# Kernel optimization log

Measured on AMD Instinct MI355X. Metric: run time of the kernel, lower is better.

Reference implementation:

```python
import jax, jax.numpy as jnp
import numpy as np

B, N, F, H, K, C = 2048, 62, 512, 128, 2, 2
EPS_BN = 1e-5
EPS_NORM = 1e-10
N_TRIL = N * (N + 1) // 2  # 1953, tril_indices incl. diagonal
FC_SIZES = [H * N, H * N // 2, H * N // 4, H * N // 8, C]  # [7936,3968,1984,992,2]


def setup_inputs() -> dict:
    key = jax.random.key(0)
    ks = jax.random.split(key, 16)
    inp = {
        "x": jax.random.normal(ks[0], (B, N, F), jnp.float32),
        "edge_weight": jax.random.uniform(ks[1], (N_TRIL,), jnp.float32),
        "bn_gamma": jnp.ones((F,), jnp.float32),
        "bn_beta": jnp.zeros((F,), jnp.float32),
        # xavier_normal for SGConv lin
        "lin_w": jax.random.normal(ks[2], (H, F), jnp.float32) * (2.0 / (F + H)) ** 0.5,
        "lin_b": jnp.zeros((H,), jnp.float32),
    }
    for i in range(4):
        fan_in, fan_out = FC_SIZES[i], FC_SIZES[i + 1]
        inp[f"fc{i}_w"] = jax.random.normal(ks[3 + i], (fan_out, fan_in), jnp.float32) * (2.0 / (fan_in + fan_out)) ** 0.5
        inp[f"fc{i}_b"] = jnp.zeros((fan_out,), jnp.float32)
    return inp


def _normalized_adj(edge_weight):
    """Build symmetric dense adjacency from tril params, normalize_matrix
    (relu + sym deg-norm), then SGConv.norm (D^-1/2 A D^-1/2; self-loops are
    already on the diagonal so add_remaining_self_loops is a no-op)."""
    xs, ys = np.tril_indices(N)
    Wm = jnp.zeros((N, N), jnp.float32).at[xs, ys].set(edge_weight)
    Wm = Wm + Wm.T - jnp.diag(jnp.diag(Wm))
    A = jax.nn.relu(Wm)
    dinv = jax.lax.rsqrt(A.sum(1) + EPS_NORM)
    A = dinv[:, None] * A * dinv[None, :]
    # SGConv normalization: deg = scatter_add over rows -> row sums
    deg = A.sum(1)
    dis = jnp.where(deg > 0, deg ** -0.5, 0.0)
    return dis[:, None] * A * dis[None, :]


def reference(x, edge_weight, bn_gamma, bn_beta, lin_w, lin_b,
              fc0_w, fc0_b, fc1_w, fc1_b, fc2_w, fc2_b, fc3_w, fc3_b):
    A = _normalized_adj(edge_weight)  # [N, N], shared across batch
    # BatchNorm1d over feature channels, stats over (batch, node) dims (train mode)
    mean = x.mean((0, 1))
    var = x.var((0, 1))
    h = (x - mean) * jax.lax.rsqrt(var + EPS_BN) * bn_gamma + bn_beta  # [B,N,F]
    # K-hop SGConv propagation == dense matmul with shared normalized adjacency
    for _ in range(K):
        h = jnp.einsum('ij,bjf->bif', A, h)
    h = h @ lin_w.T + lin_b           # [B, N, H]
    h = h.reshape(B, N * H)           # node-major flatten, matches x.view(batch,-1)
    # dropout is identity in eval mode
    for W, b in ((fc0_w, fc0_b), (fc1_w, fc1_b), (fc2_w, fc2_b)):
        h = jax.nn.relu(h @ W.T + b)
    return h @ fc3_w.T + fc3_b        # [B, C]
```

## Files before the change

kernel.cpp:

```cpp
#include <hip/hip_runtime.h>

typedef _Float16 f16;
typedef __attribute__((ext_vector_type(4))) _Float16 f16x4;
typedef __attribute__((ext_vector_type(8))) _Float16 f16x8;
typedef __attribute__((ext_vector_type(4))) float f32x4;

#define DEVI static __device__ __forceinline__

DEVI void async_copy16(const f16* g, f16* l) {
  __builtin_amdgcn_global_load_lds(
      (const __attribute__((address_space(1))) void*)g,
      (__attribute__((address_space(3))) void*)l, 16, 0, 0);
}

#define MEMPIN asm volatile("" ::: "memory")
#define RBAR __builtin_amdgcn_s_barrier()

__global__ __launch_bounds__(1024) void k_adj(const float* __restrict__ ew, float* __restrict__ out)
{
  __shared__ float sW[62][64];
  __shared__ float sT[62][64];
  __shared__ float d[62];
  const int tid = threadIdx.x;
  for (int idx = tid; idx < 62 * 62; idx += 1024) {
    int i = idx / 62, j = idx % 62;
    float w = (j <= i) ? ew[i * (i + 1) / 2 + j] : ew[j * (j + 1) / 2 + i];
    sW[i][j] = fmaxf(w, 0.f);
  }
  __syncthreads();
  if (tid < 62) {
    float s = 0.f;
    for (int j = 0; j < 62; j++) s += sW[tid][j];
    d[tid] = rsqrtf(s + 1e-10f);
  }
  __syncthreads();
  for (int idx = tid; idx < 62 * 62; idx += 1024) {
    int i = idx / 62, j = idx % 62;
    sW[i][j] *= d[i] * d[j];
  }
  __syncthreads();
  if (tid < 62) {
    float s = 0.f;
    for (int j = 0; j < 62; j++) s += sW[tid][j];
    d[tid] = (s > 0.f) ? rsqrtf(s) : 0.f;
  }
  __syncthreads();
  for (int idx = tid; idx < 62 * 62; idx += 1024) {
    int i = idx / 62, j = idx % 62;
    sW[i][j] *= d[i] * d[j];
  }
  __syncthreads();
  for (int idx = tid; idx < 62 * 64; idx += 1024) {
    int i = idx >> 6, j = idx & 63;
    float s = 0.f;
    if (j < 62) {
      for (int k = 0; k < 62; k++) s += sW[i][k] * sW[k][j];
    }
    sT[i][j] = s;
    out[idx] = s;
  }
  __syncthreads();
  if (tid < 62) {
    float s = 0.f;
    for (int j = 0; j < 62; j++) s += sT[tid][j];
    out[62 * 64 + tid] = s;
  }
}

__global__ __launch_bounds__(1024) void k_bnstats(const float* __restrict__ X, float* __restrict__ part)
{
  const int tid = threadIdx.x;
  const int c4 = (tid & 127) << 2;
  const int rg = tid >> 7;
  float sx = 0, sy = 0, sz = 0, sw = 0, qx = 0, qy = 0, qz = 0, qw = 0;
  const long r0 = (long)blockIdx.x * 496 + rg;
  for (int i = 0; i < 62; i++) {
    const float4 v = *(const float4*)(X + (r0 + 8 * i) * 512 + c4);
    sx += v.x; sy += v.y; sz += v.z; sw += v.w;
    qx += v.x * v.x; qy += v.y * v.y; qz += v.z * v.z; qw += v.w * v.w;
  }
  __shared__ float red[1024][8];
  red[tid][0] = sx; red[tid][1] = sy; red[tid][2] = sz; red[tid][3] = sw;
  red[tid][4] = qx; red[tid][5] = qy; red[tid][6] = qz; red[tid][7] = qw;
  __syncthreads();
  if (tid < 128) {
    float acc8[8];
#pragma unroll
    for (int j = 0; j < 8; j++) acc8[j] = 0.f;
#pragma unroll
    for (int g = 0; g < 8; g++)
#pragma unroll
      for (int j = 0; j < 8; j++) acc8[j] += red[g * 128 + tid][j];
    float* p = part + (long)blockIdx.x * 1024;
#pragma unroll
    for (int j = 0; j < 4; j++) p[c4 + j] = acc8[j];
#pragma unroll
    for (int j = 0; j < 4; j++) p[512 + c4 + j] = acc8[4 + j];
  }
}

__global__ __launch_bounds__(512) void k_bnfin(const float* __restrict__ part, const float* __restrict__ g,
                                               const float* __restrict__ be, float* __restrict__ ssb)
{
  const int c = threadIdx.x;
  float s = 0.f, q = 0.f;
  for (int b = 0; b < 256; b++) {
    s += part[b * 1024 + c];
    q += part[b * 1024 + 512 + c];
  }
  const float inv = 1.f / 126976.f;
  const float mean = s * inv;
  const float var = q * inv - mean * mean;
  const float sc = g[c] * rsqrtf(var + 1e-5f);
  ssb[c] = sc;
  ssb[512 + c] = be[c] - mean * sc;
}

__global__ __launch_bounds__(256) void k_foldw1(const float* __restrict__ lw, const float* __restrict__ ssb,
                                                f16* __restrict__ w1h, float* __restrict__ b1p)
{
  const int h = blockIdx.x;
  const int tid = threadIdx.x;
  float partl = 0.f;
  for (int f = tid; f < 512; f += 256) {
    const float w = lw[h * 512 + f];
    w1h[h * 512 + f] = (f16)(w * ssb[f]);
    partl += w * ssb[512 + f];
  }
  __shared__ float red[256];
  red[tid] = partl;
  __syncthreads();
  for (int s = 128; s; s >>= 1) {
    if (tid < s) red[tid] += red[tid + s];
    __syncthreads();
  }
  if (tid == 0) b1p[h] = red[0];
}

__global__ __launch_bounds__(256) void k_cvtw(const float* __restrict__ src, f16* __restrict__ dst,
                                              int N, int K, int Npad, int Kpad)
{
  const long total4 = (long)Npad * Kpad / 4;
  const int kp4 = Kpad >> 2;
  for (long i = (long)blockIdx.x * 256 + threadIdx.x; i < total4; i += (long)gridDim.x * 256) {
    const long n = i / kp4;
    const int k = (int)(i % kp4) << 2;
    f16x4 h;
    if (n < N && k < K) {
      const float4 v = *(const float4*)(src + n * K + k);
      h[0] = (f16)v.x; h[1] = (f16)v.y; h[2] = (f16)v.z; h[3] = (f16)v.w;
    } else {
      h[0] = (f16)0.f; h[1] = (f16)0.f; h[2] = (f16)0.f; h[3] = (f16)0.f;
    }
    *(f16x4*)(dst + i * 4) = h;
  }
}

__global__ __launch_bounds__(256, 2) void k_linprop(
    const float* __restrict__ X, const f16* __restrict__ Bw,
    const float* __restrict__ A2, const float* __restrict__ b1p,
    const float* __restrict__ lb, f16* __restrict__ Z)
{
  __shared__ f16 smem[128 * 128];
  __shared__ float sA2[62 * 64];
  __shared__ float sR[62];
  __shared__ float sB1[128];
  __shared__ float sLB[128];
  f16* sA = smem;
  f16* sB = smem + 8192;
  const int tid = threadIdx.x;
  const int lane = tid & 63;
  const int wave = tid >> 6;
  const int wr = wave >> 1, wc = wave & 1;
  const long rowA0 = (long)blockIdx.x * 124;

  for (int i = tid; i < 992; i += 256)
    *(float4*)&sA2[i * 4] = *(const float4*)(A2 + i * 4);
  if (tid < 62) sR[tid] = A2[3968 + tid];
  if (tid < 128) sB1[tid] = b1p[tid];
  if (tid >= 128) sLB[tid - 128] = lb[tid - 128];

  const int srow = tid >> 3;
  const int scolb = (tid & 7) << 4;
  const int gcolb = scolb ^ ((srow & 7) << 4);
  const f16* gB = Bw + (long)srow * 512 + (gcolb >> 1);
  f16* lB = sB + srow * 64 + (scolb >> 1);

  const int ac4 = tid & 15;
  const int ar0 = tid >> 4;
  const int aswz = (ar0 & 7) << 4;
  char* lAbase = (char*)sA + ar0 * 128 + ((ac4 * 8) ^ aswz);

  const int frow = lane & 15;
  const int kb = (lane >> 4) << 4;
  const int rswz = (lane & 7) << 4;

  f32x4 acc[4][4] = {};

  for (int kt = 0; kt < 512; kt += 64) {
#pragma unroll
    for (int i = 0; i < 8; i++) {
      long rr = rowA0 + ar0 + 16 * i;
      if (rr > 126975) rr = 126975;
      const float4 v = *(const float4*)(X + rr * 512 + kt + ac4 * 4);
      f16x4 hh;
      hh[0] = (f16)v.x; hh[1] = (f16)v.y; hh[2] = (f16)v.z; hh[3] = (f16)v.w;
      *(f16x4*)(lAbase + 16 * i * 128) = hh;
    }
#pragma unroll
    for (int i = 0; i < 4; i++)
      async_copy16(gB + kt + (long)i * (32 * 512), lB + i * 2048);
    __syncthreads();
#pragma unroll
    for (int kk = 0; kk < 2; kk++) {
      f16x8 af[4], bf[4];
#pragma unroll
      for (int m = 0; m < 4; m++) {
        const int row = wr * 64 + m * 16 + frow;
        af[m] = *(const f16x8*)((const char*)sA + row * 128 + ((kk * 64 + kb) ^ rswz));
      }
#pragma unroll
      for (int n = 0; n < 4; n++) {
        const int row = wc * 64 + n * 16 + frow;
        bf[n] = *(const f16x8*)((const char*)sB + row * 128 + ((kk * 64 + kb) ^ rswz));
      }
#pragma unroll
      for (int m = 0; m < 4; m++)
#pragma unroll
        for (int n = 0; n < 4; n++)
          acc[m][n] = __builtin_amdgcn_mfma_f32_16x16x32_f16(af[m], bf[n], acc[m][n], 0, 0, 0);
    }
    __syncthreads();
  }

  const int crow = wr * 64 + ((lane >> 4) << 2);
  const int ccol = wc * 64 + (lane & 15);
#pragma unroll
  for (int n = 0; n < 4; n++)
#pragma unroll
    for (int m = 0; m < 4; m++)
#pragma unroll
      for (int r = 0; r < 4; r++)
        smem[(crow + m * 16 + r) * 128 + ccol + n * 16] = (f16)acc[m][n][r];
  __syncthreads();

  const int h = tid & 127;
  const int g = tid >> 7;
  float yc[62];
#pragma unroll
  for (int j = 0; j < 62; j++) yc[j] = (float)smem[(g * 62 + j) * 128 + h];
  const float bh1 = sB1[h];
  const float bh2 = sLB[h];
  f16* zp = Z + ((long)blockIdx.x * 2 + g) * 7936 + h;
  for (int n = 0; n < 62; n++) {
    float s = 0.f;
#pragma unroll
    for (int j = 0; j < 62; j++) s += sA2[n * 64 + j] * yc[j];
    zp[n * 128] = (f16)(s + sR[n] * bh1 + bh2);
  }
}

template <int LOOPN, int MT, int NT, int KS>
__global__ __launch_bounds__(512, 2) void k_fc8(
    const f16* __restrict__ A, const f16* __restrict__ Bw, f16* __restrict__ P,
    const int K, const int kslice, const int PLD)
{
  __shared__ f16 sA[2][256 * 64];
  __shared__ f16 sB[2][256 * 64];
  const int tid = threadIdx.x;
  const int bid = blockIdx.x;
  const int xcd = bid & 7, ii = bid >> 3;
  int nt, mt, ks;
  if constexpr (NT == 16) {
    nt = xcd * 2 + (ii & 1); mt = (ii >> 1) & (MT - 1); ks = ii >> 4;
  } else {
    nt = xcd; mt = ii & (MT - 1); ks = ii >> 3;
  }
  const long rowA0 = (long)mt * 256;
  const long rowB0 = (long)nt * 256;
  const long k0 = (long)ks * kslice;

  const int srow = tid >> 3;
  const int scolb = (tid & 7) << 4;
  const int gcolb = scolb ^ ((srow & 7) << 4);
  const f16* gA = A + (rowA0 + srow) * (long)K + k0 + (gcolb >> 1);
  const f16* gB = Bw + (rowB0 + srow) * (long)K + k0 + (gcolb >> 1);

#define SGA(d, q, kt) async_copy16(gA + (kt) + (long)(q) * 64 * K, &sA[d][0] + (q) * 4096 + tid * 8)
#define SGB(d, q, kt) async_copy16(gB + (kt) + (long)(q) * 64 * K, &sB[d][0] + (q) * 4096 + tid * 8)

  const int lane = tid & 63;
  const int wave = tid >> 6;
  const int wr = wave >> 2;
  const int wc = wave & 3;
  const int frow = lane & 15;
  const int kb = (lane >> 4) << 4;
  const int rsw = (frow & 7) << 4;

  f32x4 acc[8][4] = {};
  f16x8 af[4][2], bf[4][2];

#define RDA(d, mh) do { _Pragma("unroll") for (int m_ = 0; m_ < 4; m_++) {                      \
    const int row_ = wr * 128 + (mh) * 64 + m_ * 16 + frow;                                     \
    af[m_][0] = *(const f16x8*)((const char*)&sA[d][0] + row_ * 128 + (kb ^ rsw));              \
    af[m_][1] = *(const f16x8*)((const char*)&sA[d][0] + row_ * 128 + ((64 + kb) ^ rsw)); } } while (0)
#define RDB(d) do { _Pragma("unroll") for (int n_ = 0; n_ < 4; n_++) {                          \
    const int row_ = wc * 64 + n_ * 16 + frow;                                                  \
    bf[n_][0] = *(const f16x8*)((const char*)&sB[d][0] + row_ * 128 + (kb ^ rsw));              \
    bf[n_][1] = *(const f16x8*)((const char*)&sB[d][0] + row_ * 128 + ((64 + kb) ^ rsw)); } } while (0)
#define QUAD(mh, nh) do { _Pragma("unroll") for (int m_ = 0; m_ < 4; m_++)                      \
    _Pragma("unroll") for (int n_ = 0; n_ < 2; n_++) {                                          \
      acc[(mh)*4+m_][(nh)*2+n_] = __builtin_amdgcn_mfma_f32_16x16x32_f16(af[m_][0], bf[(nh)*2+n_][0], acc[(mh)*4+m_][(nh)*2+n_], 0, 0, 0); \
      acc[(mh)*4+m_][(nh)*2+n_] = __builtin_amdgcn_mfma_f32_16x16x32_f16(af[m_][1], bf[(nh)*2+n_][1], acc[(mh)*4+m_][(nh)*2+n_], 0, 0, 0); } } while (0)
#define VMW8 asm volatile("s_waitcnt vmcnt(8)" ::: "memory")
#define VMW0 asm volatile("s_waitcnt vmcnt(0)" ::: "memory")
#define PRIO1 __builtin_amdgcn_s_setprio(1)
#define PRIO0 __builtin_amdgcn_s_setprio(0)

  SGA(0, 0, 0); SGA(0, 2, 0); SGB(0, 0, 0); SGB(0, 1, 0);
  SGA(0, 1, 0); SGA(0, 3, 0); SGB(0, 2, 0); SGB(0, 3, 0);
  SGA(1, 0, 64); SGA(1, 2, 64); SGB(1, 0, 64); SGB(1, 1, 64);
  SGA(1, 1, 64); SGA(1, 3, 64); SGB(1, 2, 64); SGB(1, 3, 64);

  for (int t = 0; t < LOOPN; ++t) {
    const long kt2 = (long)(t + 1) * 128;
    VMW8; MEMPIN; RBAR; MEMPIN;
    RDA(0, 0); RDB(0);
    PRIO1; QUAD(0, 0); PRIO0;
    MEMPIN; RBAR; MEMPIN;
    SGA(0, 0, kt2); SGA(0, 2, kt2); SGB(0, 0, kt2); SGB(0, 1, kt2);
    QUAD(0, 1);
    RDA(0, 1);
    QUAD(1, 0);
    MEMPIN; RBAR; MEMPIN;
    SGA(0, 1, kt2); SGA(0, 3, kt2); SGB(0, 2, kt2); SGB(0, 3, kt2);
    QUAD(1, 1);
    VMW8; MEMPIN; RBAR; MEMPIN;
    RDA(1, 0); RDB(1);
    PRIO1; QUAD(0, 0); PRIO0;
    MEMPIN; RBAR; MEMPIN;
    SGA(1, 0, kt2 + 64); SGA(1, 2, kt2 + 64); SGB(1, 0, kt2 + 64); SGB(1, 1, kt2 + 64);
    QUAD(0, 1);
    RDA(1, 1);
    QUAD(1, 0);
    MEMPIN; RBAR; MEMPIN;
    SGA(1, 1, kt2 + 64); SGA(1, 3, kt2 + 64); SGB(1, 2, kt2 + 64); SGB(1, 3, kt2 + 64);
    QUAD(1, 1);
  }
  VMW8; MEMPIN; RBAR; MEMPIN;
  RDA(0, 0); RDB(0);
  PRIO1; QUAD(0, 0); QUAD(0, 1); PRIO0;
  RDA(0, 1);
  PRIO1; QUAD(1, 0); QUAD(1, 1); PRIO0;
  VMW0; MEMPIN; RBAR; MEMPIN;
  RDA(1, 0); RDB(1);
  PRIO1; QUAD(0, 0); QUAD(0, 1); PRIO0;
  RDA(1, 1);
  PRIO1; QUAD(1, 0); QUAD(1, 1); PRIO0;

  f16* Pp = P + (long)ks * 2048 * PLD;
#pragma unroll
  for (int mi = 0; mi < 8; mi++) {
    const long r0 = rowA0 + wr * 128 + (mi >> 2) * 64 + (mi & 3) * 16 + ((lane >> 4) << 2);
#pragma unroll
    for (int n = 0; n < 4; n++) {
      const long col = rowB0 + wc * 64 + n * 16 + (lane & 15);
#pragma unroll
      for (int r = 0; r < 4; r++)
        Pp[(r0 + r) * PLD + col] = (f16)acc[mi][n][r];
    }
  }
#undef SGA
#undef SGB
#undef RDA
#undef RDB
#undef QUAD
#undef VMW8
#undef VMW0
#undef PRIO1
#undef PRIO0
}

template <int S>
__global__ __launch_bounds__(256) void k_fixs(const f16* __restrict__ P, const float* __restrict__ b,
                                              f16* __restrict__ C, int N, int realN)
{
  const long total = 2048L * N;
  const int mask = N - 1;
  const long stride = (long)gridDim.x * 256 * 8;
  for (long i = ((long)blockIdx.x * 256 + threadIdx.x) * 8; i < total; i += stride) {
    float s[8];
#pragma unroll
    for (int j = 0; j < 8; j++) s[j] = 0.f;
#pragma unroll
    for (int ps = 0; ps < S; ps++) {
      const f16x8 p = *(const f16x8*)(P + (long)ps * total + i);
#pragma unroll
      for (int j = 0; j < 8; j++) s[j] += (float)p[j];
    }
    const int col = (int)(i & mask);
    f16x8 o;
#pragma unroll
    for (int j = 0; j < 8; j++) {
      const int c = col + j;
      const float bb = (c < realN) ? b[c] : 0.f;
      o[j] = (f16)fmaxf(s[j] + bb, 0.f);
    }
    *(f16x8*)(C + i) = o;
  }
}

template <int RELU, int KS>
__global__ __launch_bounds__(256, 2) void k_gemm_f16(
    const f16* __restrict__ A, const f16* __restrict__ B,
    const float* __restrict__ bias, f16* __restrict__ C,
    int N, int K, int realN)
{
  __shared__ f16 sA[128 * 64];
  __shared__ f16 sB[128 * 64];
  const int tid = threadIdx.x;
  const int lane = tid & 63;
  const int wave = tid >> 6;
  const int wr = wave >> 1, wc = wave & 1;
  const int bid = blockIdx.x;
  const int xcd = bid & 7, idx = bid >> 3;
  const long rowA0 = (long)(xcd * 2 + (idx & 1)) * 128;
  long rowB0;
  int ks;
  if constexpr (KS == 2) {
    rowB0 = (long)((idx >> 1) & 7) * 128;
    ks = idx >> 4;
  } else {
    rowB0 = (long)(idx >> 1) * 128;
    ks = 0;
  }
  const int kslice = K / KS;
  const long k0 = (long)ks * kslice;

  const int srow = tid >> 3;
  const int scolb = (tid & 7) << 4;
  const int gcolb = scolb ^ ((srow & 7) << 4);
  const f16* gA = A + (rowA0 + srow) * (long)K + k0 + (gcolb >> 1);
  const f16* gB = B + (rowB0 + srow) * (long)K + k0 + (gcolb >> 1);
  f16* lA = sA + srow * 64 + (scolb >> 1);
  f16* lB = sB + srow * 64 + (scolb >> 1);
  const long rstep = 32L * K;

  const int frow = lane & 15;
  const int kb = (lane >> 4) << 4;
  const int rswz = (lane & 7) << 4;

  f32x4 acc[4][4] = {};

  for (int kt = 0; kt < kslice; kt += 64) {
#pragma unroll
    for (int i = 0; i < 4; i++) {
      async_copy16(gA + kt + i * rstep, lA + i * 2048);
      async_copy16(gB + kt + i * rstep, lB + i * 2048);
    }
    __syncthreads();
#pragma unroll
    for (int kk = 0; kk < 2; kk++) {
      f16x8 af[4], bf[4];
#pragma unroll
      for (int m = 0; m < 4; m++) {
        const int row = wr * 64 + m * 16 + frow;
        af[m] = *(const f16x8*)((const char*)sA + row * 128 + ((kk * 64 + kb) ^ rswz));
      }
#pragma unroll
      for (int n = 0; n < 4; n++) {
        const int row = wc * 64 + n * 16 + frow;
        bf[n] = *(const f16x8*)((const char*)sB + row * 128 + ((kk * 64 + kb) ^ rswz));
      }
#pragma unroll
      for (int m = 0; m < 4; m++)
#pragma unroll
        for (int n = 0; n < 4; n++)
          acc[m][n] = __builtin_amdgcn_mfma_f32_16x16x32_f16(af[m], bf[n], acc[m][n], 0, 0, 0);
    }
    __syncthreads();
  }

  const int crow = wr * 64 + ((lane >> 4) << 2);
  const int ccol = wc * 64 + (lane & 15);
  if constexpr (KS == 1) {
#pragma unroll
    for (int n = 0; n < 4; n++) {
      const int col = (int)rowB0 + ccol + n * 16;
      const float bb = (col < realN) ? bias[col] : 0.f;
#pragma unroll
      for (int m = 0; m < 4; m++) {
        const long gr = rowA0 + crow + m * 16;
#pragma unroll
        for (int r = 0; r < 4; r++) {
          float v = acc[m][n][r] + bb;
          if (RELU) v = fmaxf(v, 0.f);
          C[(gr + r) * N + col] = (f16)v;
        }
      }
    }
  } else {
    f16* Pp = C + (long)ks * 2048 * N;
#pragma unroll
    for (int n = 0; n < 4; n++) {
      const long col = rowB0 + ccol + n * 16;
#pragma unroll
      for (int m = 0; m < 4; m++) {
        const long gr = rowA0 + crow + m * 16;
#pragma unroll
        for (int r = 0; r < 4; r++)
          Pp[(gr + r) * N + col] = (f16)acc[m][n][r];
      }
    }
  }
}

__global__ __launch_bounds__(256) void k_fc3(const f16* __restrict__ H, const float* __restrict__ W,
                                             const float* __restrict__ b, float* __restrict__ out)
{
  const int row = blockIdx.x * 4 + (threadIdx.x >> 6);
  const int lane = threadIdx.x & 63;
  const f16* h = H + (long)row * 1024;
  float a0 = 0.f, a1 = 0.f;
  for (int k = lane; k < 992; k += 64) {
    const float v = (float)h[k];
    a0 += v * W[k];
    a1 += v * W[992 + k];
  }
  for (int off = 32; off; off >>= 1) {
    a0 += __shfl_down(a0, off);
    a1 += __shfl_down(a1, off);
  }
  if (lane == 0) {
    out[row * 2 + 0] = a0 + b[0];
    out[row * 2 + 1] = a1 + b[1];
  }
}

extern "C" void kernel_launch(void* const* d_in, const int* in_sizes, int n_in,
                              void* d_out, int out_size, void* d_ws, size_t ws_size,
                              hipStream_t stream)
{
  const float* x    = (const float*)d_in[0];
  const float* ew   = (const float*)d_in[1];
  const float* bng  = (const float*)d_in[2];
  const float* bnb  = (const float*)d_in[3];
  const float* linw = (const float*)d_in[4];
  const float* linb = (const float*)d_in[5];
  const float* w0   = (const float*)d_in[6];
  const float* b0   = (const float*)d_in[7];
  const float* w1   = (const float*)d_in[8];
  const float* b1   = (const float*)d_in[9];
  const float* w2   = (const float*)d_in[10];
  const float* b2   = (const float*)d_in[11];
  const float* w3   = (const float*)d_in[12];
  const float* b3   = (const float*)d_in[13];
  float* out = (float*)d_out;
  char* ws = (char*)d_ws;

  constexpr size_t oA2  = 0;
  constexpr size_t oSS  = 16384;
  constexpr size_t oB1P = 20480;
  constexpr size_t oW1H = 20992;
  constexpr size_t oP   = 152064;
  constexpr size_t oACC = oP;
  constexpr size_t oZ   = 33706496;
  constexpr size_t oW0H = 66212352;
  constexpr size_t WS_NEED = 131224064;
  constexpr size_t oH0  = oZ;
  constexpr size_t oW1F = oZ + 16777216;
  constexpr size_t oH1  = 67260928;
  constexpr size_t oW2F = 75649536;
  constexpr size_t oH2  = 79843840;
  if (ws_size < WS_NEED) return;

  float* A2  = (float*)(ws + oA2);
  float* acc = (float*)(ws + oACC);
  float* ssb = (float*)(ws + oSS);
  float* b1p = (float*)(ws + oB1P);
  f16* w1h = (f16*)(ws + oW1H);
  f16* P   = (f16*)(ws + oP);
  f16* Z   = (f16*)(ws + oZ);
  f16* w0h = (f16*)(ws + oW0H);
  f16* h0  = (f16*)(ws + oH0);
  f16* w1f = (f16*)(ws + oW1F);
  f16* h1  = (f16*)(ws + oH1);
  f16* w2f = (f16*)(ws + oW2F);
  f16* h2  = (f16*)(ws + oH2);

  k_adj<<<1, 1024, 0, stream>>>(ew, A2);
  k_bnstats<<<256, 1024, 0, stream>>>(x, acc);
  k_bnfin<<<1, 512, 0, stream>>>(acc, bng, bnb, ssb);
  k_foldw1<<<128, 256, 0, stream>>>(linw, ssb, w1h, b1p);
  k_cvtw<<<1024, 256, 0, stream>>>(w0, w0h, 3968, 7936, 4096, 7936);
  k_linprop<<<1024, 256, 0, stream>>>(x, w1h, A2, b1p, linb, Z);
  k_fc8<30, 8, 16, 2><<<256, 512, 0, stream>>>(Z, w0h, P, 7936, 3968, 4096);
  k_fixs<2><<<2048, 256, 0, stream>>>(P, b0, h0, 4096, 3968);
  k_cvtw<<<512, 256, 0, stream>>>(w1, w1f, 1984, 3968, 2048, 4096);
  k_cvtw<<<256, 256, 0, stream>>>(w2, w2f, 992, 1984, 1024, 2048);
  k_fc8<7, 8, 8, 4><<<256, 512, 0, stream>>>(h0, w1f, P, 4096, 1024, 2048);
  k_fixs<4><<<1024, 256, 0, stream>>>(P, b1, h1, 2048, 1984);
  k_gemm_f16<1, 2><<<256, 256, 0, stream>>>(h1, w2f, b2, P, 1024, 2048, 992);
  k_fixs<2><<<512, 256, 0, stream>>>(P, b2, h2, 1024, 992);
  k_fc3<<<512, 256, 0, stream>>>(h2, w3, b3, out);
}
```

Before: 465.1 us.

## Merge small kernels into co-scheduled launches and fuse final split-K reduction into fc3

Merges the adjacency build into the BN-stats launch as an extra block, folds the fc0 weight conversion into the linprop launch as extra blocks, and merges the fc0 split-K fixup with the fc1/fc2 weight conversions into one launch. The last split-K reduction plus bias and ReLU is folded into the fc3 dot-product kernel, dropping one kernel and the h2 buffer. The aim is fewer launches and more overlap between independent work. The linprop launch bound changes to 3 blocks per SM, which may limit registers, and the BN kernel now reserves LDS for the adjacency arrays.

```diff
diff --git a/kernel.cpp b/kernel.cpp
--- a/kernel.cpp
+++ b/kernel.cpp
@@ -16,12 +16,45 @@
 #define MEMPIN asm volatile("" ::: "memory")
 #define RBAR __builtin_amdgcn_s_barrier()
 
-__global__ __launch_bounds__(1024) void k_adj(const float* __restrict__ ew, float* __restrict__ out)
-{
+__global__ __launch_bounds__(1024) void k_bnadj(const float* __restrict__ X, float* __restrict__ part,
+                                                const float* __restrict__ ew, float* __restrict__ A2out)
+{
+  __shared__ float red[1024][8];
   __shared__ float sW[62][64];
   __shared__ float sT[62][64];
   __shared__ float d[62];
   const int tid = threadIdx.x;
+
+  if (blockIdx.x < 256) {
+    const int c4 = (tid & 127) << 2;
+    const int rg = tid >> 7;
+    float sx = 0, sy = 0, sz = 0, sw = 0, qx = 0, qy = 0, qz = 0, qw = 0;
+    const long r0 = (long)blockIdx.x * 496 + rg;
+    for (int i = 0; i < 62; i++) {
+      const float4 v = *(const float4*)(X + (r0 + 8 * i) * 512 + c4);
+      sx += v.x; sy += v.y; sz += v.z; sw += v.w;
+      qx += v.x * v.x; qy += v.y * v.y; qz += v.z * v.z; qw += v.w * v.w;
+    }
+    red[tid][0] = sx; red[tid][1] = sy; red[tid][2] = sz; red[tid][3] = sw;
+    red[tid][4] = qx; red[tid][5] = qy; red[tid][6] = qz; red[tid][7] = qw;
+    __syncthreads();
+    if (tid < 128) {
+      float acc8[8];
+#pragma unroll
+      for (int j = 0; j < 8; j++) acc8[j] = 0.f;
+#pragma unroll
+      for (int g = 0; g < 8; g++)
+#pragma unroll
+        for (int j = 0; j < 8; j++) acc8[j] += red[g * 128 + tid][j];
+      float* p = part + (long)blockIdx.x * 1024;
+#pragma unroll
+      for (int j = 0; j < 4; j++) p[c4 + j] = acc8[j];
+#pragma unroll
+      for (int j = 0; j < 4; j++) p[512 + c4 + j] = acc8[4 + j];
+    }
+    return;
+  }
+
   for (int idx = tid; idx < 62 * 62; idx += 1024) {
     int i = idx / 62, j = idx % 62;
     float w = (j <= i) ? ew[i * (i + 1) / 2 + j] : ew[j * (j + 1) / 2 + i];
@@ -57,45 +90,13 @@
       for (int k = 0; k < 62; k++) s += sW[i][k] * sW[k][j];
     }
     sT[i][j] = s;
-    out[idx] = s;
+    A2out[idx] = s;
   }
   __syncthreads();
   if (tid < 62) {
     float s = 0.f;
     for (int j = 0; j < 62; j++) s += sT[tid][j];
-    out[62 * 64 + tid] = s;
-  }
-}
-
-__global__ __launch_bounds__(1024) void k_bnstats(const float* __restrict__ X, float* __restrict__ part)
-{
-  const int tid = threadIdx.x;
-  const int c4 = (tid & 127) << 2;
-  const int rg = tid >> 7;
-  float sx = 0, sy = 0, sz = 0, sw = 0, qx = 0, qy = 0, qz = 0, qw = 0;
-  const long r0 = (long)blockIdx.x * 496 + rg;
-  for (int i = 0; i < 62; i++) {
-    const float4 v = *(const float4*)(X + (r0 + 8 * i) * 512 + c4);
-    sx += v.x; sy += v.y; sz += v.z; sw += v.w;
-    qx += v.x * v.x; qy += v.y * v.y; qz += v.z * v.z; qw += v.w * v.w;
-  }
-  __shared__ float red[1024][8];
-  red[tid][0] = sx; red[tid][1] = sy; red[tid][2] = sz; red[tid][3] = sw;
-  red[tid][4] = qx; red[tid][5] = qy; red[tid][6] = qz; red[tid][7] = qw;
-  __syncthreads();
-  if (tid < 128) {
-    float acc8[8];
-#pragma unroll
-    for (int j = 0; j < 8; j++) acc8[j] = 0.f;
-#pragma unroll
-    for (int g = 0; g < 8; g++)
-#pragma unroll
-      for (int j = 0; j < 8; j++) acc8[j] += red[g * 128 + tid][j];
-    float* p = part + (long)blockIdx.x * 1024;
-#pragma unroll
-    for (int j = 0; j < 4; j++) p[c4 + j] = acc8[j];
-#pragma unroll
-    for (int j = 0; j < 4; j++) p[512 + c4 + j] = acc8[4 + j];
+    A2out[62 * 64 + tid] = s;
   }
 }
 
@@ -137,12 +138,12 @@
   if (tid == 0) b1p[h] = red[0];
 }
 
-__global__ __launch_bounds__(256) void k_cvtw(const float* __restrict__ src, f16* __restrict__ dst,
-                                              int N, int K, int Npad, int Kpad)
+DEVI void cvt_body(const float* __restrict__ src, f16* __restrict__ dst,
+                   int N, int K, int Npad, int Kpad, int bix, int nblk)
 {
   const long total4 = (long)Npad * Kpad / 4;
   const int kp4 = Kpad >> 2;
-  for (long i = (long)blockIdx.x * 256 + threadIdx.x; i < total4; i += (long)gridDim.x * 256) {
+  for (long i = (long)bix * 256 + threadIdx.x; i < total4; i += (long)nblk * 256) {
     const long n = i / kp4;
     const int k = (int)(i % kp4) << 2;
     f16x4 h;
@@ -156,16 +157,23 @@
   }
 }
 
-__global__ __launch_bounds__(256, 2) void k_linprop(
+__global__ __launch_bounds__(256, 3) void k_linprop_cvt(
     const float* __restrict__ X, const f16* __restrict__ Bw,
     const float* __restrict__ A2, const float* __restrict__ b1p,
-    const float* __restrict__ lb, f16* __restrict__ Z)
+    const float* __restrict__ lb, f16* __restrict__ Z,
+    const float* __restrict__ w0, f16* __restrict__ w0h)
 {
   __shared__ f16 smem[128 * 128];
   __shared__ float sA2[62 * 64];
   __shared__ float sR[62];
   __shared__ float sB1[128];
   __shared__ float sLB[128];
+
+  if (blockIdx.x >= 1024) {
+    cvt_body(w0, w0h, 3968, 7936, 4096, 7936, blockIdx.x - 1024, 1024);
+    return;
+  }
+
   f16* sA = smem;
   f16* sB = smem + 8192;
   const int tid = threadIdx.x;
@@ -382,13 +390,13 @@
 }
 
 template <int S>
-__global__ __launch_bounds__(256) void k_fixs(const f16* __restrict__ P, const float* __restrict__ b,
-                                              f16* __restrict__ C, int N, int realN)
+DEVI void fix_body(const f16* __restrict__ P, const float* __restrict__ b,
+                   f16* __restrict__ C, int N, int realN, int bix, int nblk)
 {
   const long total = 2048L * N;
   const int mask = N - 1;
-  const long stride = (long)gridDim.x * 256 * 8;
-  for (long i = ((long)blockIdx.x * 256 + threadIdx.x) * 8; i < total; i += stride) {
+  const long stride = (long)nblk * 256 * 8;
+  for (long i = ((long)bix * 256 + threadIdx.x) * 8; i < total; i += stride) {
     float s[8];
 #pragma unroll
     for (int j = 0; j < 8; j++) s[j] = 0.f;
@@ -408,6 +416,24 @@
     }
     *(f16x8*)(C + i) = o;
   }
+}
+
+template <int S>
+__global__ __launch_bounds__(256) void k_fixs(const f16* __restrict__ P, const float* __restrict__ b,
+                                              f16* __restrict__ C, int N, int realN)
+{
+  fix_body<S>(P, b, C, N, realN, blockIdx.x, gridDim.x);
+}
+
+__global__ __launch_bounds__(256) void k_fixcvt(const f16* __restrict__ P, const float* __restrict__ b0,
+                                                f16* __restrict__ h0,
+                                                const float* __restrict__ w1, f16* __restrict__ w1f,
+                                                const float* __restrict__ w2, f16* __restrict__ w2f)
+{
+  const int bx = blockIdx.x;
+  if (bx < 2048)       fix_body<2>(P, b0, h0, 4096, 3968, bx, 2048);
+  else if (bx < 2560)  cvt_body(w1, w1f, 1984, 3968, 2048, 4096, bx - 2048, 512);
+  else                 cvt_body(w2, w2f, 992, 1984, 1024, 2048, bx - 2560, 256);
 }
 
 template <int RELU, int KS>
@@ -515,15 +541,17 @@
   }
 }
 
-__global__ __launch_bounds__(256) void k_fc3(const f16* __restrict__ H, const float* __restrict__ W,
-                                             const float* __restrict__ b, float* __restrict__ out)
+__global__ __launch_bounds__(256) void k_fc3p(const f16* __restrict__ P, const float* __restrict__ b2,
+                                              const float* __restrict__ W, const float* __restrict__ b,
+                                              float* __restrict__ out)
 {
   const int row = blockIdx.x * 4 + (threadIdx.x >> 6);
   const int lane = threadIdx.x & 63;
-  const f16* h = H + (long)row * 1024;
+  const f16* p0 = P + (long)row * 1024;
+  const f16* p1 = P + 2048L * 1024 + (long)row * 1024;
   float a0 = 0.f, a1 = 0.f;
   for (int k = lane; k < 992; k += 64) {
-    const float v = (float)h[k];
+    const float v = fmaxf((float)p0[k] + (float)p1[k] + b2[k], 0.f);
     a0 += v * W[k];
     a1 += v * W[992 + k];
   }
@@ -571,7 +599,6 @@
   constexpr size_t oW1F = oZ + 16777216;
   constexpr size_t oH1  = 67260928;
   constexpr size_t oW2F = 75649536;
-  constexpr size_t oH2  = 79843840;
   if (ws_size < WS_NEED) return;
 
   float* A2  = (float*)(ws + oA2);
@@ -586,21 +613,15 @@
   f16* w1f = (f16*)(ws + oW1F);
   f16* h1  = (f16*)(ws + oH1);
   f16* w2f = (f16*)(ws + oW2F);
-  f16* h2  = (f16*)(ws + oH2);
-
-  k_adj<<<1, 1024, 0, stream>>>(ew, A2);
-  k_bnstats<<<256, 1024, 0, stream>>>(x, acc);
+
+  k_bnadj<<<257, 1024, 0, stream>>>(x, acc, ew, A2);
   k_bnfin<<<1, 512, 0, stream>>>(acc, bng, bnb, ssb);
   k_foldw1<<<128, 256, 0, stream>>>(linw, ssb, w1h, b1p);
-  k_cvtw<<<1024, 256, 0, stream>>>(w0, w0h, 3968, 7936, 4096, 7936);
-  k_linprop<<<1024, 256, 0, stream>>>(x, w1h, A2, b1p, linb, Z);
+  k_linprop_cvt<<<2048, 256, 0, stream>>>(x, w1h, A2, b1p, linb, Z, w0, w0h);
   k_fc8<30, 8, 16, 2><<<256, 512, 0, stream>>>(Z, w0h, P, 7936, 3968, 4096);
-  k_fixs<2><<<2048, 256, 0, stream>>>(P, b0, h0, 4096, 3968);
-  k_cvtw<<<512, 256, 0, stream>>>(w1, w1f, 1984, 3968, 2048, 4096);
-  k_cvtw<<<256, 256, 0, stream>>>(w2, w2f, 992, 1984, 1024, 2048);
+  k_fixcvt<<<2816, 256, 0, stream>>>(P, b0, h0, w1, w1f, w2, w2f);
   k_fc8<7, 8, 8, 4><<<256, 512, 0, stream>>>(h0, w1f, P, 4096, 1024, 2048);
   k_fixs<4><<<1024, 256, 0, stream>>>(P, b1, h1, 2048, 1984);
   k_gemm_f16<1, 2><<<256, 256, 0, stream>>>(h1, w2f, b2, P, 1024, 2048, 992);
-  k_fixs<2><<<512, 256, 0, stream>>>(P, b2, h2, 1024, 992);
-  k_fc3<<<512, 256, 0, stream>>>(h2, w3, b3, out);
-}
+  k_fc3p<<<512, 256, 0, stream>>>(P, b2, w3, b3, out);
+}
```

New measurement: 409.5 us (median of 2 runs). 1.14x faster.
